# Performance work log

Hardware: AMD Instinct MI355X
Metric: run time of the kernel (lower is better)

The kernel has to match this reference:

```python
import jax, jax.numpy as jnp
import numpy as np

C = 16          # number of classes
LAM = 25.0      # lambda_param (invariance)
MU = 25.0       # mu_param (variance)
NU = 1.0        # nu_param (covariance)
ALPHA = 50.0    # alpha_param (class-discriminative margin & weight)
EPS = 1e-4


def setup_inputs() -> dict:
    key = jax.random.key(0)
    k1, k2, k3 = jax.random.split(key, 3)
    N, D = 32768, 256
    z_a = jax.random.normal(k1, (N, D), dtype=jnp.float32)
    z_b = jax.random.normal(k2, (N, D), dtype=jnp.float32)
    labels = jax.random.randint(k3, (N,), 0, C)
    return {"z_a": z_a, "z_b": z_b, "labels": labels}


def _class_stats(x, labels):
    # counts [C], mean [C,D], unbiased var [C,D] via one segmented pass
    ones = jnp.ones(x.shape[0], x.dtype)
    counts = jax.ops.segment_sum(ones, labels, num_segments=C)
    s = jax.ops.segment_sum(x, labels, num_segments=C)
    sq = jax.ops.segment_sum(x * x, labels, num_segments=C)
    mean = s / counts[:, None]
    var = (sq - counts[:, None] * mean * mean) / (counts[:, None] - 1.0)
    return counts, mean, var


def _variance_loss(var):
    # mean over classes of mean_D relu(1 - std); D equal per class -> global mean
    std = jnp.sqrt(var + EPS)
    return jnp.mean(jax.nn.relu(1.0 - std))


def _covariance_loss(x, labels, counts, mean):
    D = x.shape[1]
    e = x - mean[labels]  # centered per class

    def per_class(c):
        w = (labels == c).astype(x.dtype)
        em = e * w[:, None]
        cov = em.T @ em / (counts[c] - 1.0)  # [D, D]
        off = (cov * cov).sum() - (jnp.diagonal(cov) ** 2).sum()
        return off / D

    return jnp.mean(jax.lax.map(per_class, jnp.arange(C)))


def _class_disc_loss(mean_a, mean_b):
    m = 0.5 * (mean_a + mean_b)               # [C, D]
    diff = m[:, None, :] - m[None, :, :]      # [C, C, D]
    d2 = jnp.sum(diff * diff, axis=-1)        # [C, C]
    mask = jnp.triu(jnp.ones((C, C), bool), 1)
    dist = jnp.sqrt(jnp.where(mask, d2, 1.0))  # safe sqrt off-mask
    pen = jnp.where(mask, jax.nn.relu(ALPHA - dist) ** 2, 0.0)
    npairs = C * (C - 1) // 2
    return pen.sum() / npairs


def reference(z_a, z_b, labels):
    inv_loss = jnp.mean((z_a - z_b) ** 2)
    ca, ma, va = _class_stats(z_a, labels)
    cb, mb, vb = _class_stats(z_b, labels)
    var_loss = 0.5 * (_variance_loss(va) + _variance_loss(vb))
    cov_loss = 0.5 * (_covariance_loss(z_a, labels, ca, ma)
                      + _covariance_loss(z_b, labels, cb, mb))
    class_loss = _class_disc_loss(ma, mb)
    return LAM * inv_loss + MU * var_loss + NU * cov_loss + ALPHA * class_loss
```

## Files before the change

### kernel.cpp

```cpp
#include <hip/hip_runtime.h>
#include <math.h>

#define N_ROWS 32768
#define D 256
#define C 16

#define WS_SUMS_A 0
#define WS_SQ_A   4096
#define WS_SUMS_B 8192
#define WS_SQ_B   12288
#define WS_INV    16384
#define WS_COV    16385
#define WS_COUNTS 16392
#define WS_CURSOR 16408
#define WS_POFFP  16424
#define WS_EOFF   16448
#define WS_INVP   16512
#define WS_COVP   17024
#define WS_PERM   17920
#define WS_ZERO_FLOATS 16408

#define WS_PSUM   50688
#define WS_HPART  181760
#define WS_GPART2 189952
#define GP_TILE2P 2048
#define NTASK     10
#define NSPLIT    8
#define KC        2
#define GP_PER_SPLIT2P (NTASK * C * 2 * GP_TILE2P)
#define RIDX_CAP  1024
#define NEED_A ((size_t)(WS_GPART2 + NSPLIT * GP_PER_SPLIT2P) * 4)

typedef __attribute__((ext_vector_type(8))) __bf16 bf16x8;
typedef __attribute__((ext_vector_type(16))) float f32x16;

__device__ inline unsigned bf16_rne(float f) {
    unsigned u = __float_as_uint(f);
    return (u + 0x7fffu + ((u >> 16) & 1u)) >> 16;
}
__device__ inline unsigned pack_bf16(float lo, float hi) {
    return bf16_rne(lo) | (bf16_rne(hi) << 16);
}
__device__ inline int img_base4(int c, int kd) {
    return c * 20 + ((kd + ((c >> 1) & 12)) & 12);
}
__device__ inline int img_base2(int c, int kd) {
    return c * 20 + ((kd + ((c >> 1) & 12)) & 14);
}
__device__ inline void task_rc(int w, int& r, int& c) {
    if (w < 4)      { r = 0; c = w; }
    else if (w < 7) { r = 1; c = w - 3; }
    else if (w < 9) { r = 2; c = w - 5; }
    else            { r = 3; c = 3; }
}


__global__ __launch_bounds__(512) void k_hist2(const int* __restrict__ labels,
                                               int* __restrict__ hpart) {
    __shared__ int h[C];
    const int t = threadIdx.x;
    if (t < C) h[t] = 0;
    __syncthreads();
    atomicAdd(&h[labels[blockIdx.x * 512 + t]], 1);
    __syncthreads();
    if (t < C) hpart[blockIdx.x * C + t] = h[t];
}

__global__ __launch_bounds__(512) void k_scatter2(const int* __restrict__ labels,
                                                  const int* __restrict__ hpart,
                                                  int* __restrict__ counts,
                                                  int* __restrict__ poffp,
                                                  int* __restrict__ eoffp,
                                                  int* __restrict__ perm) {
    const int t = threadIdx.x;
    const int B = blockIdx.x;
    __shared__ int lh[C];
    __shared__ int tot[32][C];
    __shared__ int pre[32][C];
    __shared__ int ccnt[C], cpre[C], ceoff[C];
    const int i = B * 512 + t;
    const int lab = labels[i];
    if (t < C) lh[t] = 0;
    const int c = t & 15, seg = t >> 4;
    {
        const int p0 = 2 * seg, p1 = p0 + 1;
        const int v0 = hpart[p0 * C + c], v1 = hpart[p1 * C + c];
        tot[seg][c] = v0 + v1;
        pre[seg][c] = (p0 < B ? v0 : 0) + (p1 < B ? v1 : 0);
    }
    __syncthreads();
    const int lr = atomicAdd(&lh[lab], 1);
    if (t < C) {
        int s1 = 0, s2 = 0;
        #pragma unroll
        for (int g = 0; g < 32; ++g) { s1 += tot[g][t]; s2 += pre[g][t]; }
        ccnt[t] = s1;
        cpre[t] = s2;
    }
    __syncthreads();
    if (t == 0) {
        int off = 0, po = 0;
        for (int cc = 0; cc < C; ++cc) {
            ceoff[cc] = off;
            if (B == 0) { eoffp[cc] = off; poffp[cc] = po; counts[cc] = ccnt[cc]; }
            off += ccnt[cc];
            po += (ccnt[cc] + 31) >> 5;
        }
        if (B == 0) { eoffp[C] = off; poffp[C] = po; }
    }
    __syncthreads();
    perm[ceoff[lab] + cpre[lab] + lr] = i;
}

__global__ __launch_bounds__(640) void k_gram7(const float* __restrict__ za,
                                               const float* __restrict__ zb,
                                               const int* __restrict__ perm,
                                               const int* __restrict__ counts,
                                               const int* __restrict__ poffp,
                                               const int* __restrict__ eoffp,
                                               float* __restrict__ ws) {
    const int t = threadIdx.x;
    const int split = blockIdx.x;
    const int cls = blockIdx.y, inp = blockIdx.z;
    const float* X = inp ? zb : za;
    const int cnt = counts[cls];
    const int eoff = eoffp[cls];
    const int nsteps = poffp[cls + 1] - poffp[cls];
    const int chunk = (nsteps + NSPLIT - 1) / NSPLIT;
    const int sb = split * chunk;
    const int se = min(sb + chunk, nsteps);

    __shared__ __align__(16) unsigned img[2][5120];
    __shared__ float sstats[512];
    __shared__ float redI[8];
    __shared__ int ridx[RIDX_CAP];

    for (int i = t; i < 512; i += 640) sstats[i] = 0.f;
    const int nl = (se > sb) ? (se - sb) * 32 : 0;
    for (int i = t; i < nl && i < RIDX_CAP; i += 640) {
        const int gr = sb * 32 + i;
        ridx[i] = (gr < cnt) ? perm[eoff + gr] : -1;
    }
    __syncthreads();

    auto rowidx = [&](int li) -> int {
        if (li < RIDX_CAP) return ridx[li];
        const int gr = sb * 32 + li;
        return (gr < cnt) ? perm[eoff + gr] : -1;
    };

    const int lane = t & 63, w = t >> 6;
    const int cg = lane & 31, q = lane >> 5;
    int tr, tc;
    task_rc(w, tr, tc);
    const bool stg = (t < 512);

    const int lc = 4 * (t & 63);
    const int kp0 = 2 * ((t >> 6) & 7);

    f32x16 acc[2][2];
    #pragma unroll
    for (int i = 0; i < 2; ++i)
        #pragma unroll
        for (int j = 0; j < 2; ++j) acc[i][j] = 0.0f;

    float s1r[4] = {0.f, 0.f, 0.f, 0.f};
    float s2r[4] = {0.f, 0.f, 0.f, 0.f};
    float accI = 0.f;
    float4 f0[2], f1[2];
    float4 g0[2], g1[2];

    auto load_regs = [&](int s) {
        #pragma unroll
        for (int it = 0; it < 2; ++it) {
            const int li = (s - sb) * 32 + 2 * (kp0 + it);
            const int r0 = rowidx(li), r1 = rowidx(li + 1);
            f0[it] = (r0 >= 0) ? *(const float4*)(X + (size_t)r0 * D + lc)
                               : make_float4(0.f, 0.f, 0.f, 0.f);
            f1[it] = (r1 >= 0) ? *(const float4*)(X + (size_t)r1 * D + lc)
                               : make_float4(0.f, 0.f, 0.f, 0.f);
            if (inp == 0) {
                g0[it] = (r0 >= 0) ? *(const float4*)(zb + (size_t)r0 * D + lc)
                                   : make_float4(0.f, 0.f, 0.f, 0.f);
                g1[it] = (r1 >= 0) ? *(const float4*)(zb + (size_t)r1 * D + lc)
                                   : make_float4(0.f, 0.f, 0.f, 0.f);
            }
        }
    };
    auto pack_store = [&](int buf) {
        unsigned pw[4][2];
        #pragma unroll
        for (int it = 0; it < 2; ++it) {
            pw[0][it] = pack_bf16(f0[it].x, f1[it].x);
            pw[1][it] = pack_bf16(f0[it].y, f1[it].y);
            pw[2][it] = pack_bf16(f0[it].z, f1[it].z);
            pw[3][it] = pack_bf16(f0[it].w, f1[it].w);
        }
        #pragma unroll
        for (int d = 0; d < 4; ++d)
            *(uint2*)&img[buf][img_base2(lc + d, kp0)] = make_uint2(pw[d][0], pw[d][1]);
        #pragma unroll
        for (int it = 0; it < 2; ++it) {
            s1r[0] += f0[it].x + f1[it].x; s2r[0] += f0[it].x * f0[it].x + f1[it].x * f1[it].x;
            s1r[1] += f0[it].y + f1[it].y; s2r[1] += f0[it].y * f0[it].y + f1[it].y * f1[it].y;
            s1r[2] += f0[it].z + f1[it].z; s2r[2] += f0[it].z * f0[it].z + f1[it].z * f1[it].z;
            s1r[3] += f0[it].w + f1[it].w; s2r[3] += f0[it].w * f0[it].w + f1[it].w * f1[it].w;
        }
        if (inp == 0) {
            #pragma unroll
            for (int it = 0; it < 2; ++it) {
                float d0, d1;
                d0 = f0[it].x - g0[it].x; d1 = f1[it].x - g1[it].x; accI += d0 * d0 + d1 * d1;
                d0 = f0[it].y - g0[it].y; d1 = f1[it].y - g1[it].y; accI += d0 * d0 + d1 * d1;
                d0 = f0[it].z - g0[it].z; d1 = f1[it].z - g1[it].z; accI += d0 * d0 + d1 * d1;
                d0 = f0[it].w - g0[it].w; d1 = f1[it].w - g1[it].w; accI += d0 * d0 + d1 * d1;
            }
        }
    };
    auto frag = [&](int buf, int col, int kd) -> bf16x8 {
        return *(const bf16x8*)&img[buf][img_base4(col, kd)];
    };

    if (sb < se) {
        if (stg) { load_regs(sb); pack_store(0); }
        __syncthreads();
        for (int s = sb; s < se; ++s) {
            const int buf = (s - sb) & 1;
            const bool more = (s + 1 < se);
            if (stg && more) load_regs(s + 1);
            #pragma unroll
            for (int h = 0; h < 2; ++h) {
                const int kd = h * 8 + q * 4;
                bf16x8 a0 = frag(buf, tr * 64 + cg, kd);
                bf16x8 a1 = frag(buf, tr * 64 + 32 + cg, kd);
                bf16x8 b0, b1;
                if (tr == tc) { b0 = a0; b1 = a1; }
                else {
                    b0 = frag(buf, tc * 64 + cg, kd);
                    b1 = frag(buf, tc * 64 + 32 + cg, kd);
                }
                acc[0][0] = __builtin_amdgcn_mfma_f32_32x32x16_bf16(a0, b0, acc[0][0], 0, 0, 0);
                acc[0][1] = __builtin_amdgcn_mfma_f32_32x32x16_bf16(a0, b1, acc[0][1], 0, 0, 0);
                acc[1][0] = __builtin_amdgcn_mfma_f32_32x32x16_bf16(a1, b0, acc[1][0], 0, 0, 0);
                acc[1][1] = __builtin_amdgcn_mfma_f32_32x32x16_bf16(a1, b1, acc[1][1], 0, 0, 0);
            }
            if (stg && more) pack_store(buf ^ 1);
            __syncthreads();
        }
    }

    unsigned* gp = (unsigned*)ws + WS_GPART2 + (size_t)split * GP_PER_SPLIT2P
                 + (((size_t)cls * 2 + inp) * NTASK + w) * GP_TILE2P;
    #pragma unroll
    for (int i = 0; i < 2; ++i)
        #pragma unroll
        for (int r = 0; r < 16; ++r) {
            const int row = i * 32 + (r & 3) + 8 * (r >> 2) + 4 * q;
            gp[row * 32 + cg] = pack_bf16(acc[i][0][r], acc[i][1][r]);
        }

    if (inp == 0 && stg) {
        float v = accI;
        for (int o = 32; o > 0; o >>= 1) v += __shfl_down(v, o, 64);
        if (lane == 0) redI[w] = v;
    }
    if (stg) {
        #pragma unroll
        for (int d = 0; d < 4; ++d) {
            atomicAdd(&sstats[lc + d],       s1r[d]);
            atomicAdd(&sstats[256 + lc + d], s2r[d]);
        }
    }
    __syncthreads();
    if (inp == 0 && t == 0) {
        float s = 0.f;
        #pragma unroll
        for (int k = 0; k < 8; ++k) s += redI[k];
        ws[WS_INVP + split * C + cls] = s;
    }
    const size_t pbase = (((size_t)split * C + cls) * 2 + inp) * 512;
    for (int i = t; i < 512; i += 640) ws[WS_PSUM + pbase + i] = sstats[i];
}

__global__ __launch_bounds__(256) void k_cov4(const int* __restrict__ counts,
                                              float* __restrict__ ws) {
    const int t = threadIdx.x;
    const int w = blockIdx.x / KC, k0 = blockIdx.x % KC;
    int tr, tc;
    task_rc(w, tr, tc);
    const int cls = blockIdx.y, inp = blockIdx.z;
    const int cnt = counts[cls];
    const float fc = (float)cnt;
    const float cinv = 1.f / fc, uinv = 1.f / (fc - 1.f);
    const float wgt = (tr == tc) ? 1.f : 2.f;
    __shared__ float Mr[64], Mc[64];
    if (t < 64) {
        float s = 0.f;
        #pragma unroll
        for (int sp = 0; sp < NSPLIT; ++sp)
            s += ws[WS_PSUM + (((size_t)sp * C + cls) * 2 + inp) * 512 + tr * 64 + t];
        Mr[t] = s * cinv;
    } else if (t < 128) {
        const int u = t - 64;
        float s = 0.f;
        #pragma unroll
        for (int sp = 0; sp < NSPLIT; ++sp)
            s += ws[WS_PSUM + (((size_t)sp * C + cls) * 2 + inp) * 512 + tc * 64 + u];
        Mc[u] = s * cinv;
    }
    if (w == 0 && k0 == 0) {
        float s1 = 0.f, s2 = 0.f;
        #pragma unroll
        for (int sp = 0; sp < NSPLIT; ++sp) {
            const size_t pb = WS_PSUM + (((size_t)sp * C + cls) * 2 + inp) * 512;
            s1 += ws[pb + t];
            s2 += ws[pb + 256 + t];
        }
        ws[(inp ? WS_SUMS_B : WS_SUMS_A) + cls * D + t] = s1;
        ws[(inp ? WS_SQ_B   : WS_SQ_A)   + cls * D + t] = s2;
    }
    __syncthreads();

    const int e0 = k0 * 1024 + t * 4;
    const unsigned* gp0 = (const unsigned*)ws + WS_GPART2
                        + (((size_t)cls * 2 + inp) * NTASK + w) * GP_TILE2P + e0;
    uint4 u4[NSPLIT];
    #pragma unroll
    for (int sp = 0; sp < NSPLIT; ++sp)
        u4[sp] = *(const uint4*)(gp0 + (size_t)sp * GP_PER_SPLIT2P);

    float glo[4] = {0.f, 0.f, 0.f, 0.f};
    float ghi[4] = {0.f, 0.f, 0.f, 0.f};
    #pragma unroll
    for (int sp = 0; sp < NSPLIT; ++sp) {
        const unsigned* uu = (const unsigned*)&u4[sp];
        #pragma unroll
        for (int j = 0; j < 4; ++j) {
            glo[j] += __uint_as_float(uu[j] << 16);
            ghi[j] += __uint_as_float(uu[j] & 0xffff0000u);
        }
    }
    const int row = e0 >> 5, c0 = e0 & 31;
    const float mr = Mr[row];
    float local = 0.f;
    #pragma unroll
    for (int j = 0; j < 4; ++j) {
        const float clo = (glo[j] - fc * mr * Mc[c0 + j]) * uinv;
        const float chi = (ghi[j] - fc * mr * Mc[c0 + j + 32]) * uinv;
        if (!(tr == tc && row == c0 + j))      local += wgt * clo * clo;
        if (!(tr == tc && row == c0 + j + 32)) local += wgt * chi * chi;
    }
    for (int o = 32; o > 0; o >>= 1) local += __shfl_down(local, o, 64);
    __shared__ float red[4];
    if ((t & 63) == 0) red[t >> 6] = local;
    __syncthreads();
    if (t == 0)
        ws[WS_COVP + (((size_t)inp * C + cls) * NTASK + w) * KC + k0] =
            red[0] + red[1] + red[2] + red[3];
}

__global__ __launch_bounds__(512) void k_hist(const int* __restrict__ labels,
                                              int* __restrict__ counts) {
    __shared__ int h[C];
    const int t = threadIdx.x;
    if (t < C) h[t] = 0;
    __syncthreads();
    const int i = blockIdx.x * 512 + t;
    atomicAdd(&h[labels[i]], 1);
    __syncthreads();
    if (t < C) atomicAdd(&counts[t], h[t]);
}

__global__ void k_scan(const int* __restrict__ counts, int* __restrict__ cursor,
                       int* __restrict__ poffp, int* __restrict__ eoffp) {
    if (threadIdx.x == 0) {
        int off = 0, po = 0;
        for (int c = 0; c < C; ++c) {
            cursor[c] = off;
            eoffp[c] = off;
            poffp[c] = po;
            off += counts[c];
            po += (counts[c] + 31) >> 5;
        }
        poffp[C] = po;
        eoffp[C] = off;
    }
}

__global__ __launch_bounds__(512) void k_scatter(const int* __restrict__ labels,
                                                 int* __restrict__ cursor,
                                                 int* __restrict__ perm) {
    __shared__ int lh[C];
    __shared__ int lbase[C];
    const int t = threadIdx.x;
    if (t < C) lh[t] = 0;
    __syncthreads();
    const int i = blockIdx.x * 512 + t;
    const int lab = labels[i];
    const int lr = atomicAdd(&lh[lab], 1);
    __syncthreads();
    if (t < C) lbase[t] = atomicAdd(&cursor[t], lh[t]);
    __syncthreads();
    perm[lbase[lab] + lr] = i;
}

__global__ __launch_bounds__(256) void k_stats(const float* __restrict__ za,
                                               const float* __restrict__ zb,
                                               const int* __restrict__ labels,
                                               float* __restrict__ ws) {
    const int t = threadIdx.x;
    __shared__ float S[4][C * D];
    __shared__ int lab[512];
    for (int i = t; i < 4 * C * D; i += 256) ((float*)S)[i] = 0.f;
    const int r0 = blockIdx.x * 512;
    for (int i = t; i < 512; i += 256) lab[i] = labels[r0 + i];
    __syncthreads();
    float invp = 0.f;
    #pragma unroll 4
    for (int rr = 0; rr < 512; ++rr) {
        const int l = lab[rr];
        const float a = za[(size_t)(r0 + rr) * D + t];
        const float b = zb[(size_t)(r0 + rr) * D + t];
        const float dd = a - b;
        invp += dd * dd;
        S[0][l * D + t] += a;
        S[1][l * D + t] += a * a;
        S[2][l * D + t] += b;
        S[3][l * D + t] += b * b;
    }
    __syncthreads();
    #pragma unroll
    for (int c = 0; c < C; ++c) {
        atomicAdd(&ws[WS_SUMS_A + c * D + t], S[0][c * D + t]);
        atomicAdd(&ws[WS_SQ_A   + c * D + t], S[1][c * D + t]);
        atomicAdd(&ws[WS_SUMS_B + c * D + t], S[2][c * D + t]);
        atomicAdd(&ws[WS_SQ_B   + c * D + t], S[3][c * D + t]);
    }
    for (int o = 32; o > 0; o >>= 1) invp += __shfl_down(invp, o, 64);
    if ((t & 63) == 0) atomicAdd(&ws[WS_INV], invp);
}

#define STR 20
#define KB 32
__global__ __launch_bounds__(256) void k_gram_slow(const float* __restrict__ za,
                                                   const float* __restrict__ zb,
                                                   const int* __restrict__ perm,
                                                   const int* __restrict__ counts,
                                                   float* __restrict__ ws) {
    const int t = threadIdx.x;
    const int tile = blockIdx.x;
    const int tx = tile >> 1, ty = (tile + 1) >> 1;
    const int cls = blockIdx.y;
    const int inp = blockIdx.z;
    const float* X = inp ? zb : za;
    const float* sums = ws + (inp ? WS_SUMS_B : WS_SUMS_A) + cls * D;
    int offs = 0;
    for (int c = 0; c < cls; ++c) offs += counts[c];
    const int cnt = counts[cls];
    const int cm0 = tx * 128, cn0 = ty * 128;
    __shared__ __align__(16) unsigned lds[2][256 * STR];
    const int p = t >> 5, cq = t & 31;
    const int lane = t & 63, w = t >> 6;
    const int wr = w & 1, wc = w >> 1;
    const int cg = lane & 31, q = lane >> 5;
    f32x16 acc[2][2];
    #pragma unroll
    for (int i = 0; i < 2; ++i)
        #pragma unroll
        for (int j = 0; j < 2; ++j) acc[i][j] = 0.0f;
    const int nsteps = (cnt + KB - 1) / KB;
    auto stage = [&](int buf, int k0) {
        #pragma unroll
        for (int ch = 0; ch < 2; ++ch) {
            const int gc = (ch ? cn0 : cm0) + 4 * cq;
            #pragma unroll
            for (int sub = 0; sub < 2; ++sub) {
                const int rr = sub * 16 + 2 * p;
                const int r0 = k0 + rr, r1 = r0 + 1;
                float4 v0 = make_float4(0.f, 0.f, 0.f, 0.f), v1 = v0;
                if (r0 < cnt) v0 = *(const float4*)(X + (size_t)perm[offs + r0] * D + gc);
                if (r1 < cnt) v1 = *(const float4*)(X + (size_t)perm[offs + r1] * D + gc);
                unsigned* dst = &lds[buf][(ch * 128 + 4 * cq) * STR + (rr >> 1)];
                dst[0 * STR] = pack_bf16(v0.x, v1.x);
                dst[1 * STR] = pack_bf16(v0.y, v1.y);
                dst[2 * STR] = pack_bf16(v0.z, v1.z);
                dst[3 * STR] = pack_bf16(v0.w, v1.w);
            }
        }
    };
    auto frag = [&](int buf, int colbase, int h) -> bf16x8 {
        return *(const bf16x8*)&lds[buf][(colbase + cg) * STR + h * 8 + q * 4];
    };
    stage(0, 0);
    for (int s = 0; s < nsteps; ++s) {
        __syncthreads();
        const int buf = s & 1;
        if (s + 1 < nsteps) stage(buf ^ 1, (s + 1) * KB);
        #pragma unroll
        for (int h = 0; h < 2; ++h) {
            bf16x8 a0 = frag(buf, wr * 64, h);
            bf16x8 a1 = frag(buf, wr * 64 + 32, h);
            bf16x8 b0 = frag(buf, 128 + wc * 64, h);
            bf16x8 b1 = frag(buf, 128 + wc * 64 + 32, h);
            acc[0][0] = __builtin_amdgcn_mfma_f32_32x32x16_bf16(a0, b0, acc[0][0], 0, 0, 0);
            acc[0][1] = __builtin_amdgcn_mfma_f32_32x32x16_bf16(a0, b1, acc[0][1], 0, 0, 0);
            acc[1][0] = __builtin_amdgcn_mfma_f32_32x32x16_bf16(a1, b0, acc[1][0], 0, 0, 0);
            acc[1][1] = __builtin_amdgcn_mfma_f32_32x32x16_bf16(a1, b1, acc[1][1], 0, 0, 0);
        }
    }
    const float fc = (float)cnt;
    const float cinv = 1.f / fc, uinv = 1.f / (fc - 1.f);
    const float wgt = (tx == ty) ? 1.f : 2.f;
    float local = 0.f;
    #pragma unroll
    for (int i = 0; i < 2; ++i) {
        #pragma unroll
        for (int j = 0; j < 2; ++j) {
            const int gn = cn0 + wc * 64 + j * 32 + (lane & 31);
            const float mn = sums[gn] * cinv;
            #pragma unroll
            for (int r = 0; r < 16; ++r) {
                const int row = (r & 3) + 8 * (r >> 2) + 4 * q;
                const int gm = cm0 + wr * 64 + i * 32 + row;
                const float cov = (acc[i][j][r] - fc * (sums[gm] * cinv) * mn) * uinv;
                if (gm != gn) local += wgt * cov * cov;
            }
        }
    }
    for (int o = 32; o > 0; o >>= 1) local += __shfl_down(local, o, 64);
    if (lane == 0) atomicAdd(&ws[WS_COV], local);
}

__global__ __launch_bounds__(256) void k_final(const float* __restrict__ ws,
                                               float* __restrict__ out,
                                               int fast) {
    __shared__ float M[C * D];
    __shared__ float redv[4], redi[4], redc[4], redp[4];
    const int t = threadIdx.x;
    const int* counts = (const int*)ws + WS_COUNTS;

    float vsum = 0.f;
    for (int idx = t; idx < 2 * C * D; idx += 256) {
        const int inp = idx >> 12;
        const int cd = idx & 4095;
        const int c = cd >> 8;
        const float cnt = (float)counts[c];
        const float s  = ws[(inp ? WS_SUMS_B : WS_SUMS_A) + cd];
        const float sq = ws[(inp ? WS_SQ_B   : WS_SQ_A)   + cd];
        const float mean = s / cnt;
        const float var = (sq - cnt * mean * mean) / (cnt - 1.f);
        vsum += fmaxf(1.f - sqrtf(var + 1e-4f), 0.f);
    }
    float isum, csum;
    if (fast) {
        isum = (t < 128) ? ws[WS_INVP + t] : 0.f;
        csum = ws[WS_COVP + t] + ws[WS_COVP + 256 + t]
             + ((t < 128) ? ws[WS_COVP + 512 + t] : 0.f);
    } else {
        isum = (t == 0) ? ws[WS_INV] : 0.f;
        csum = (t == 0) ? ws[WS_COV] : 0.f;
    }
    for (int cd = t; cd < C * D; cd += 256) {
        const int c = cd >> 8;
        const float cnt = (float)counts[c];
        M[cd] = 0.5f * (ws[WS_SUMS_A + cd] + ws[WS_SUMS_B + cd]) / cnt;
    }
    for (int o = 32; o > 0; o >>= 1) {
        vsum += __shfl_down(vsum, o, 64);
        isum += __shfl_down(isum, o, 64);
        csum += __shfl_down(csum, o, 64);
    }
    if ((t & 63) == 0) {
        redv[t >> 6] = vsum; redi[t >> 6] = isum; redc[t >> 6] = csum;
    }
    __syncthreads();

    const int wv = t >> 6, ln = t & 63;
    float psum = 0.f;
    int p = 0;
    for (int i = 0; i < C; ++i) {
        for (int j = i + 1; j < C; ++j, ++p) {
            if ((p & 3) != wv) continue;
            float d2 = 0.f;
            #pragma unroll
            for (int d = ln; d < D; d += 64) {
                const float df = M[i * D + d] - M[j * D + d];
                d2 += df * df;
            }
            for (int o = 32; o > 0; o >>= 1) d2 += __shfl_down(d2, o, 64);
            if (ln == 0) {
                const float dist = sqrtf(d2);
                const float r = fmaxf(50.f - dist, 0.f);
                psum += r * r;
            }
        }
    }
    if (ln == 0) redp[wv] = psum;
    __syncthreads();

    if (t == 0) {
        const float var_loss = (redv[0] + redv[1] + redv[2] + redv[3]) / 8192.f;
        const float class_loss = (redp[0] + redp[1] + redp[2] + redp[3]) / 120.f;
        const float inv_loss = (redi[0] + redi[1] + redi[2] + redi[3]) / (float)(N_ROWS * D);
        const float cov_loss = 0.5f * (redc[0] + redc[1] + redc[2] + redc[3]) / (float)(C * D);
        out[0] = 25.f * inv_loss + 25.f * var_loss + 1.f * cov_loss + 50.f * class_loss;
    }
}

extern "C" void kernel_launch(void* const* d_in, const int* in_sizes, int n_in,
                              void* d_out, int out_size, void* d_ws, size_t ws_size,
                              hipStream_t stream) {
    const float* za = (const float*)d_in[0];
    const float* zb = (const float*)d_in[1];
    const int* labels = (const int*)d_in[2];
    float* out = (float*)d_out;
    float* ws = (float*)d_ws;
    int* wsi = (int*)d_ws;

    if (ws_size >= NEED_A) {
        k_hist2<<<64, 512, 0, stream>>>(labels, wsi + WS_HPART);
        k_scatter2<<<64, 512, 0, stream>>>(labels, wsi + WS_HPART, wsi + WS_COUNTS,
                                           wsi + WS_POFFP, wsi + WS_EOFF, wsi + WS_PERM);
        k_gram7<<<dim3(NSPLIT, C, 2), 640, 0, stream>>>(
            za, zb, wsi + WS_PERM, wsi + WS_COUNTS, wsi + WS_POFFP,
            wsi + WS_EOFF, ws);
        k_cov4<<<dim3(NTASK * KC, C, 2), 256, 0, stream>>>(wsi + WS_COUNTS, ws);
        k_final<<<1, 256, 0, stream>>>(ws, out, 1);
    } else {
        hipMemsetAsync(d_ws, 0, WS_ZERO_FLOATS * sizeof(float), stream);
        k_hist<<<64, 512, 0, stream>>>(labels, wsi + WS_COUNTS);
        k_scan<<<1, 64, 0, stream>>>(wsi + WS_COUNTS, wsi + WS_CURSOR,
                                     wsi + WS_POFFP, wsi + WS_EOFF);
        k_scatter<<<64, 512, 0, stream>>>(labels, wsi + WS_CURSOR, wsi + WS_PERM);
        k_stats<<<64, 256, 0, stream>>>(za, zb, labels, ws);
        k_gram_slow<<<dim3(3, C, 2), 256, 0, stream>>>(za, zb, wsi + WS_PERM,
                                                       wsi + WS_COUNTS, ws);
        k_final<<<1, 256, 0, stream>>>(ws, out, 0);
    }
}
```

Measured before the change: 159.1 us.

## Fold histogram into scatter kernel and split invariance loss across both inputs

Drops the separate histogram kernel. Each scatter block now recomputes the full label histogram and its own block prefix, using per-thread shared-memory counters over all 64 label chunks. This removes one launch and one global round trip, at the cost of redundant label reads in every block. The invariance-loss partner loads are also split between the za and zb gram blocks, so each handles half the rows' partner reads. The final kernel sums both sets of partials, which balances load across the two input grids.

Measured after the change: 170.3 us. 7.0% more time.

```diff
diff --git a/kernel.cpp b/kernel.cpp
--- a/kernel.cpp
+++ b/kernel.cpp
@@ -21,7 +21,6 @@
 #define WS_ZERO_FLOATS 16408
 
 #define WS_PSUM   50688
-#define WS_HPART  181760
 #define WS_GPART2 189952
 #define GP_TILE2P 2048
 #define NTASK     10
@@ -55,41 +54,39 @@
 }
 
 
-__global__ __launch_bounds__(512) void k_hist2(const int* __restrict__ labels,
-                                               int* __restrict__ hpart) {
-    __shared__ int h[C];
-    const int t = threadIdx.x;
-    if (t < C) h[t] = 0;
-    __syncthreads();
-    atomicAdd(&h[labels[blockIdx.x * 512 + t]], 1);
-    __syncthreads();
-    if (t < C) hpart[blockIdx.x * C + t] = h[t];
-}
-
-__global__ __launch_bounds__(512) void k_scatter2(const int* __restrict__ labels,
-                                                  const int* __restrict__ hpart,
+__global__ __launch_bounds__(512) void k_scatter3(const int* __restrict__ labels,
                                                   int* __restrict__ counts,
                                                   int* __restrict__ poffp,
                                                   int* __restrict__ eoffp,
                                                   int* __restrict__ perm) {
     const int t = threadIdx.x;
     const int B = blockIdx.x;
+    __shared__ int H[C][513];
+    __shared__ int Hp[C][513];
     __shared__ int lh[C];
     __shared__ int tot[32][C];
     __shared__ int pre[32][C];
     __shared__ int ccnt[C], cpre[C], ceoff[C];
-    const int i = B * 512 + t;
-    const int lab = labels[i];
+    for (int i = t; i < C * 513; i += 512) { (&H[0][0])[i] = 0; (&Hp[0][0])[i] = 0; }
     if (t < C) lh[t] = 0;
-    const int c = t & 15, seg = t >> 4;
+    __syncthreads();
+    #pragma unroll 4
+    for (int k = 0; k < 64; ++k) {
+        const int lab = labels[k * 512 + t];
+        H[lab][t]++;
+        if (k < B) Hp[lab][t]++;
+    }
+    __syncthreads();
     {
-        const int p0 = 2 * seg, p1 = p0 + 1;
-        const int v0 = hpart[p0 * C + c], v1 = hpart[p1 * C + c];
-        tot[seg][c] = v0 + v1;
-        pre[seg][c] = (p0 < B ? v0 : 0) + (p1 < B ? v1 : 0);
-    }
-    __syncthreads();
-    const int lr = atomicAdd(&lh[lab], 1);
+        const int c = t & 15, seg = t >> 4;
+        int tt = 0, pp = 0;
+        const int plo = seg * 16;
+        #pragma unroll
+        for (int p = plo; p < plo + 16; ++p) { tt += H[c][p]; pp += Hp[c][p]; }
+        tot[seg][c] = tt;
+        pre[seg][c] = pp;
+    }
+    __syncthreads();
     if (t < C) {
         int s1 = 0, s2 = 0;
         #pragma unroll
@@ -109,10 +106,13 @@
         if (B == 0) { eoffp[C] = off; poffp[C] = po; }
     }
     __syncthreads();
+    const int i = B * 512 + t;
+    const int lab = labels[i];
+    const int lr = atomicAdd(&lh[lab], 1);
     perm[ceoff[lab] + cpre[lab] + lr] = i;
 }
 
-__global__ __launch_bounds__(640) void k_gram7(const float* __restrict__ za,
+__global__ __launch_bounds__(640) void k_gram8(const float* __restrict__ za,
                                                const float* __restrict__ zb,
                                                const int* __restrict__ perm,
                                                const int* __restrict__ counts,
@@ -123,6 +123,7 @@
     const int split = blockIdx.x;
     const int cls = blockIdx.y, inp = blockIdx.z;
     const float* X = inp ? zb : za;
+    const float* Y = inp ? za : zb;
     const int cnt = counts[cls];
     const int eoff = eoffp[cls];
     const int nsteps = poffp[cls + 1] - poffp[cls];
@@ -168,7 +169,7 @@
     float s2r[4] = {0.f, 0.f, 0.f, 0.f};
     float accI = 0.f;
     float4 f0[2], f1[2];
-    float4 g0[2], g1[2];
+    float4 p0, p1;
 
     auto load_regs = [&](int s) {
         #pragma unroll
@@ -179,11 +180,11 @@
                                : make_float4(0.f, 0.f, 0.f, 0.f);
             f1[it] = (r1 >= 0) ? *(const float4*)(X + (size_t)r1 * D + lc)
                                : make_float4(0.f, 0.f, 0.f, 0.f);
-            if (inp == 0) {
-                g0[it] = (r0 >= 0) ? *(const float4*)(zb + (size_t)r0 * D + lc)
-                                   : make_float4(0.f, 0.f, 0.f, 0.f);
-                g1[it] = (r1 >= 0) ? *(const float4*)(zb + (size_t)r1 * D + lc)
-                                   : make_float4(0.f, 0.f, 0.f, 0.f);
+            if (it == inp) {
+                p0 = (r0 >= 0) ? *(const float4*)(Y + (size_t)r0 * D + lc)
+                               : make_float4(0.f, 0.f, 0.f, 0.f);
+                p1 = (r1 >= 0) ? *(const float4*)(Y + (size_t)r1 * D + lc)
+                               : make_float4(0.f, 0.f, 0.f, 0.f);
             }
         }
     };
@@ -207,14 +208,17 @@
             s1r[3] += f0[it].w + f1[it].w; s2r[3] += f0[it].w * f0[it].w + f1[it].w * f1[it].w;
         }
         if (inp == 0) {
-            #pragma unroll
-            for (int it = 0; it < 2; ++it) {
-                float d0, d1;
-                d0 = f0[it].x - g0[it].x; d1 = f1[it].x - g1[it].x; accI += d0 * d0 + d1 * d1;
-                d0 = f0[it].y - g0[it].y; d1 = f1[it].y - g1[it].y; accI += d0 * d0 + d1 * d1;
-                d0 = f0[it].z - g0[it].z; d1 = f1[it].z - g1[it].z; accI += d0 * d0 + d1 * d1;
-                d0 = f0[it].w - g0[it].w; d1 = f1[it].w - g1[it].w; accI += d0 * d0 + d1 * d1;
-            }
+            float d0, d1;
+            d0 = f0[0].x - p0.x; d1 = f1[0].x - p1.x; accI += d0 * d0 + d1 * d1;
+            d0 = f0[0].y - p0.y; d1 = f1[0].y - p1.y; accI += d0 * d0 + d1 * d1;
+            d0 = f0[0].z - p0.z; d1 = f1[0].z - p1.z; accI += d0 * d0 + d1 * d1;
+            d0 = f0[0].w - p0.w; d1 = f1[0].w - p1.w; accI += d0 * d0 + d1 * d1;
+        } else {
+            float d0, d1;
+            d0 = f0[1].x - p0.x; d1 = f1[1].x - p1.x; accI += d0 * d0 + d1 * d1;
+            d0 = f0[1].y - p0.y; d1 = f1[1].y - p1.y; accI += d0 * d0 + d1 * d1;
+            d0 = f0[1].z - p0.z; d1 = f1[1].z - p1.z; accI += d0 * d0 + d1 * d1;
+            d0 = f0[1].w - p0.w; d1 = f1[1].w - p1.w; accI += d0 * d0 + d1 * d1;
         }
     };
     auto frag = [&](int buf, int col, int kd) -> bf16x8 {
@@ -259,12 +263,10 @@
             gp[row * 32 + cg] = pack_bf16(acc[i][0][r], acc[i][1][r]);
         }
 
-    if (inp == 0 && stg) {
+    if (stg) {
         float v = accI;
         for (int o = 32; o > 0; o >>= 1) v += __shfl_down(v, o, 64);
         if (lane == 0) redI[w] = v;
-    }
-    if (stg) {
         #pragma unroll
         for (int d = 0; d < 4; ++d) {
             atomicAdd(&sstats[lc + d],       s1r[d]);
@@ -272,11 +274,11 @@
         }
     }
     __syncthreads();
-    if (inp == 0 && t == 0) {
+    if (t == 0) {
         float s = 0.f;
         #pragma unroll
         for (int k = 0; k < 8; ++k) s += redI[k];
-        ws[WS_INVP + split * C + cls] = s;
+        ws[WS_INVP + (inp * NSPLIT + split) * C + cls] = s;
     }
     const size_t pbase = (((size_t)split * C + cls) * 2 + inp) * 512;
     for (int i = t; i < 512; i += 640) ws[WS_PSUM + pbase + i] = sstats[i];
@@ -553,7 +555,7 @@
     }
     float isum, csum;
     if (fast) {
-        isum = (t < 128) ? ws[WS_INVP + t] : 0.f;
+        isum = ws[WS_INVP + t];
         csum = ws[WS_COVP + t] + ws[WS_COVP + 256 + t]
              + ((t < 128) ? ws[WS_COVP + 512 + t] : 0.f);
     } else {
@@ -618,10 +620,10 @@
     int* wsi = (int*)d_ws;
 
     if (ws_size >= NEED_A) {
-        k_hist2<<<64, 512, 0, stream>>>(labels, wsi + WS_HPART);
-        k_scatter2<<<64, 512, 0, stream>>>(labels, wsi + WS_HPART, wsi + WS_COUNTS,
-                                           wsi + WS_POFFP, wsi + WS_EOFF, wsi + WS_PERM);
-        k_gram7<<<dim3(NSPLIT, C, 2), 640, 0, stream>>>(
+        k_scatter3<<<64, 512, 0, stream>>>(labels, wsi + WS_COUNTS,
+                                           wsi + WS_POFFP, wsi + WS_EOFF,
+                                           wsi + WS_PERM);
+        k_gram8<<<dim3(NSPLIT, C, 2), 640, 0, stream>>>(
             za, zb, wsi + WS_PERM, wsi + WS_COUNTS, wsi + WS_POFFP,
             wsi + WS_EOFF, ws);
         k_cov4<<<dim3(NTASK * KC, C, 2), 256, 0, stream>>>(wsi + WS_COUNTS, ws);
```
